# Optimization experiments

Hardware: AMD Instinct MI355X
Metric: run time of the kernel (lower is better)

Reference implementation:

```python
import jax, jax.numpy as jnp
import numpy as np

B, H, C, PX, PY = 2, 16, 4, 16, 16
EXTRA = 64
HD = 64
N = C * PX * PY + EXTRA


def setup_inputs() -> dict:
    key = jax.random.key(0)
    ks = jax.random.split(key, 8)
    q = jax.random.normal(ks[0], (B, H, N, HD), jnp.float32)
    k = jax.random.normal(ks[1], (B, H, N, HD), jnp.float32)
    v = jax.random.normal(ks[2], (B, H, N, HD), jnp.float32)
    # valid SE(3) world-to-camera matrices: rotation via QR (det fixed to +1)
    A = jax.random.normal(ks[3], (B, C, 3, 3), jnp.float32)
    Q, _ = jnp.linalg.qr(A)
    det = jnp.linalg.det(Q)
    Q = Q * det[..., None, None]
    t = 0.5 * jax.random.normal(ks[4], (B, C, 3), jnp.float32)
    top = jnp.concatenate([Q, t[..., None]], -1)
    bot = jnp.broadcast_to(jnp.array([0.0, 0.0, 0.0, 1.0], jnp.float32), (B, C, 1, 4))
    viewmats = jnp.concatenate([top, bot], -2)
    # pinhole intrinsics (no skew)
    fx = 300.0 + 10.0 * jax.random.uniform(ks[5], (B, C))
    fy = 300.0 + 10.0 * jax.random.uniform(ks[6], (B, C))
    z = jnp.zeros((B, C)); o = jnp.ones((B, C))
    cx = 128.0 * o; cy = 128.0 * o
    Ks = jnp.stack([jnp.stack([fx, z, cx], -1), jnp.stack([z, fy, cy], -1), jnp.stack([z, z, o], -1)], -2)
    spatial_mask = jnp.arange(N) >= EXTRA  # first EXTRA tokens are non-spatial
    return {"q": q, "k": k, "v": v, "viewmats": viewmats, "Ks": Ks,
            "spatial_mask": spatial_mask, "patches_x": PX, "patches_y": PY,
            "image_width": 256, "image_height": 256}


def _invert_SE3(T):
    R = T[..., :3, :3]; t = T[..., :3, 3]
    Rinv = jnp.swapaxes(R, -1, -2)
    tinv = -jnp.einsum('...ij,...j->...i', Rinv, t)
    top = jnp.concatenate([Rinv, tinv[..., None]], -1)
    bot = jnp.broadcast_to(jnp.array([0.0, 0.0, 0.0, 1.0], T.dtype), T.shape[:-2] + (1, 4))
    return jnp.concatenate([top, bot], -2)


def _lift(K3):
    out = jnp.zeros(K3.shape[:-2] + (4, 4), K3.dtype)
    return out.at[..., :3, :3].set(K3).at[..., 3, 3].set(1.0)


def _invert_K(K):
    fx = K[..., 0, 0]; fy = K[..., 1, 1]; cx = K[..., 0, 2]; cy = K[..., 1, 2]
    z = jnp.zeros_like(fx); o = jnp.ones_like(fx)
    return jnp.stack([jnp.stack([1.0 / fx, z, -cx / fx], -1),
                      jnp.stack([z, 1.0 / fy, -cy / fy], -1),
                      jnp.stack([z, z, o], -1)], -2)


def _transform(feats, M, cosx, sinx, cosy, siny, inverse):
    # Block-diagonal: [tiled 4x4 projmat on D/2 | RoPE-x on D/4 | RoPE-y on D/4]
    Bq, Hq, Nq, D = feats.shape
    h2 = D // 2; h4 = D // 4
    p = feats[..., :h2].reshape(Bq, Hq, Nq, h2 // 4, 4)
    p = jnp.einsum('bnij,bhnkj->bhnki', M, p).reshape(Bq, Hq, Nq, h2)

    def rope(x, c, s):
        c = c[None, None]; s = s[None, None]  # [1,1,N,nf]
        xa, xb = x[..., : x.shape[-1] // 2], x[..., x.shape[-1] // 2:]
        if inverse:
            return jnp.concatenate([c * xa - s * xb, s * xa + c * xb], -1)
        return jnp.concatenate([c * xa + s * xb, -s * xa + c * xb], -1)

    rx = rope(feats[..., h2:h2 + h4], cosx, sinx)
    ry = rope(feats[..., h2 + h4:], cosy, siny)
    return jnp.concatenate([p, rx, ry], -1)


def reference(q, k, v, viewmats, Ks, spatial_mask, patches_x, patches_y, image_width, image_height):
    D = q.shape[-1]
    Bq, Cq = viewmats.shape[:2]
    # normalized intrinsics
    fx = Ks[..., 0, 0] / image_width; fy = Ks[..., 1, 1] / image_height
    cx = Ks[..., 0, 2] / image_width - 0.5; cy = Ks[..., 1, 2] / image_height - 0.5
    z = jnp.zeros_like(fx); o = jnp.ones_like(fx)
    Kn = jnp.stack([jnp.stack([fx, z, cx], -1), jnp.stack([z, fy, cy], -1), jnp.stack([z, z, o], -1)], -2)
    P = jnp.einsum('...ij,...jk->...ik', _lift(Kn), viewmats)          # [B,C,4,4]
    P_T = jnp.swapaxes(P, -1, -2)
    P_inv = jnp.einsum('...ij,...jk->...ik', _invert_SE3(viewmats), _lift(_invert_K(Kn)))
    # RoPE tables over spatial tokens (split convention, base=100, scale=1)
    nf = D // 8
    freqs = 100.0 ** (-jnp.arange(nf, dtype=jnp.float32) / nf)
    pos_x = jnp.tile(jnp.arange(patches_x, dtype=jnp.float32), patches_y * Cq)
    pos_y = jnp.tile(jnp.repeat(jnp.arange(patches_y, dtype=jnp.float32), patches_x), Cq)
    ang_x = pos_x[:, None] * freqs; ang_y = pos_y[:, None] * freqs  # [S,nf]
    mask = spatial_mask
    S = pos_x.shape[0]
    # index of each token within the spatial-token ordering (masked scatter, vectorized)
    sidx = jnp.clip(jnp.cumsum(mask.astype(jnp.int32)) - 1, 0, S - 1)
    m = mask[:, None]
    cosx = jnp.where(m, jnp.cos(ang_x)[sidx], 1.0); sinx = jnp.where(m, jnp.sin(ang_x)[sidx], 0.0)
    cosy = jnp.where(m, jnp.cos(ang_y)[sidx], 1.0); siny = jnp.where(m, jnp.sin(ang_y)[sidx], 0.0)
    cam = sidx // (patches_x * patches_y)  # camera id per token
    I4 = jnp.eye(4, dtype=q.dtype)
    mm = mask[None, :, None, None]
    Mq = jnp.where(mm, P_T[:, cam], I4)    # [B,N,4,4]
    Mkv = jnp.where(mm, P_inv[:, cam], I4)
    Mo = jnp.where(mm, P[:, cam], I4)
    qt = _transform(q, Mq, cosx, sinx, cosy, siny, False)
    kt = _transform(k, Mkv, cosx, sinx, cosy, siny, False)
    vt = _transform(v, Mkv, cosx, sinx, cosy, siny, False)
    logits = jnp.einsum('bhqd,bhkd->bhqk', qt, kt) / jnp.sqrt(jnp.float32(D))
    attn = jax.nn.softmax(logits, axis=-1)
    out = jnp.einsum('bhqk,bhkd->bhqd', attn, vt)
    return _transform(out, Mo, cosx, sinx, cosy, siny, True)
```

## Files before the change

### kernel.cpp

```cpp
#include <hip/hip_runtime.h>
#include <math.h>

typedef _Float16 f16;
typedef _Float16 f16x8 __attribute__((ext_vector_type(8)));
typedef __fp16 h16x2 __attribute__((ext_vector_type(2)));
typedef float f32x16 __attribute__((ext_vector_type(16)));
typedef unsigned int u32;
typedef u32 u32x4 __attribute__((ext_vector_type(4)));

constexpr int Bc = 2, Hc = 16, Cc = 4, PXc = 16, PYc = 16, EXTRAc = 64, HDc = 64;
constexpr int Nc = Cc * PXc * PYc + EXTRAc;
constexpr int BH = Bc * Hc;
constexpr int KT = 64;
constexpr int NKT = Nc / KT;
constexpr int KS = 4;

constexpr size_t TENS_SZ  = (size_t)BH * Nc * HDc * 2;
constexpr size_t QF_OFF   = 0;
constexpr size_t KF_OFF   = QF_OFF + TENS_SZ;
constexpr size_t VT_OFF   = KF_OFF + TENS_SZ;
constexpr size_t PART_OFF = VT_OFF + TENS_SZ;
constexpr size_t ML_OFF   = PART_OFF + (size_t)KS * TENS_SZ;

__device__ const float FREQS[8] = {1.0f, 0.5623413252f, 0.31622776601f, 0.17782794100f,
                                   0.1f, 0.05623413252f, 0.031622776602f, 0.017782794100f};
constexpr float QSCALE = 0.125f * 1.4426950408889634f;

__device__ __forceinline__ void compute_M(float* M, const float* __restrict__ vm,
                                          const float* __restrict__ Ks3, int b, int cam, int which) {
    const float* V  = vm + (b * Cc + cam) * 16;
    const float* K3 = Ks3 + (b * Cc + cam) * 9;
    float fx = K3[0] * (1.0f / 256.0f);
    float fy = K3[4] * (1.0f / 256.0f);
    float cx = K3[2] * (1.0f / 256.0f) - 0.5f;
    float cy = K3[5] * (1.0f / 256.0f) - 0.5f;
    if (which == 2) {
        float IV[16];
        IV[0] = V[0]; IV[1] = V[4]; IV[2] = V[8];
        IV[4] = V[1]; IV[5] = V[5]; IV[6] = V[9];
        IV[8] = V[2]; IV[9] = V[6]; IV[10] = V[10];
        float tx = V[3], ty = V[7], tz = V[11];
        IV[3]  = -(IV[0] * tx + IV[1] * ty + IV[2] * tz);
        IV[7]  = -(IV[4] * tx + IV[5] * ty + IV[6] * tz);
        IV[11] = -(IV[8] * tx + IV[9] * ty + IV[10] * tz);
        IV[12] = 0.f; IV[13] = 0.f; IV[14] = 0.f; IV[15] = 1.f;
        float ifx = 1.f / fx, ify = 1.f / fy;
        float ncx = -cx * ifx, ncy = -cy * ify;
        #pragma unroll
        for (int i = 0; i < 4; ++i) {
            M[i * 4 + 0] = IV[i * 4 + 0] * ifx;
            M[i * 4 + 1] = IV[i * 4 + 1] * ify;
            M[i * 4 + 2] = IV[i * 4 + 0] * ncx + IV[i * 4 + 1] * ncy + IV[i * 4 + 2];
            M[i * 4 + 3] = IV[i * 4 + 3];
        }
    } else {
        float P[16];
        #pragma unroll
        for (int j = 0; j < 4; ++j) {
            P[0 * 4 + j] = fx * V[0 * 4 + j] + cx * V[2 * 4 + j];
            P[1 * 4 + j] = fy * V[1 * 4 + j] + cy * V[2 * 4 + j];
            P[2 * 4 + j] = V[2 * 4 + j];
            P[3 * 4 + j] = V[3 * 4 + j];
        }
        if (which == 0) {
            #pragma unroll
            for (int i = 0; i < 16; ++i) M[i] = P[i];
        } else {
            #pragma unroll
            for (int i = 0; i < 4; ++i)
                #pragma unroll
                for (int j = 0; j < 4; ++j) M[i * 4 + j] = P[j * 4 + i];
        }
    }
}

template <bool INV>
__device__ __forceinline__ void xf_seg(float* v16, int seg, int n, int b, int which,
                                       const float* __restrict__ vm, const float* __restrict__ Ks3) {
    if (n < EXTRAc) return;
    int sidx = n - EXTRAc;
    int cam = sidx >> 8;
    if (seg < 2) {
        float M[16];
        compute_M(M, vm, Ks3, b, cam, which);
        #pragma unroll
        for (int g = 0; g < 4; ++g) {
            float a0 = v16[4 * g], a1 = v16[4 * g + 1], a2 = v16[4 * g + 2], a3 = v16[4 * g + 3];
            v16[4 * g + 0] = M[0]  * a0 + M[1]  * a1 + M[2]  * a2 + M[3]  * a3;
            v16[4 * g + 1] = M[4]  * a0 + M[5]  * a1 + M[6]  * a2 + M[7]  * a3;
            v16[4 * g + 2] = M[8]  * a0 + M[9]  * a1 + M[10] * a2 + M[11] * a3;
            v16[4 * g + 3] = M[12] * a0 + M[13] * a1 + M[14] * a2 + M[15] * a3;
        }
    } else {
        float pos = (seg == 2) ? (float)(sidx & (PXc - 1)) : (float)((sidx >> 4) & (PYc - 1));
        #pragma unroll
        for (int f = 0; f < 8; ++f) {
            float s, c;
            __sincosf(pos * FREQS[f], &s, &c);
            float xa = v16[f], xb = v16[8 + f];
            if (INV) {
                v16[f]     = c * xa - s * xb;
                v16[8 + f] = s * xa + c * xb;
            } else {
                v16[f]     = c * xa + s * xb;
                v16[8 + f] = -s * xa + c * xb;
            }
        }
    }
}

__device__ __forceinline__ u32 pkh(float a, float b) {
    h16x2 r = __builtin_amdgcn_cvt_pkrtz(a, b);
    return __builtin_bit_cast(u32, r);
}

__device__ __forceinline__ void gld16(const void* g, void* l) {
    __builtin_amdgcn_global_load_lds((const __attribute__((address_space(1))) unsigned int*)g,
                                     (__attribute__((address_space(3))) unsigned int*)l, 16, 0, 0);
}

__device__ __forceinline__ f32x16 zero16() {
    f32x16 z = {0.f,0.f,0.f,0.f,0.f,0.f,0.f,0.f,0.f,0.f,0.f,0.f,0.f,0.f,0.f,0.f};
    return z;
}

__global__ void prope_xform_kernel(const float* __restrict__ q, const float* __restrict__ k,
                                   const float* __restrict__ v,
                                   const float* __restrict__ viewmats, const float* __restrict__ Ks,
                                   char* __restrict__ wsb) {
    __shared__ f16 tile[64][72];
    if (blockIdx.x < 1088) {
        int id = blockIdx.x * 256 + threadIdx.x;
        int seg = id & 3;
        int rid = id >> 2;
        int tensor = rid / (BH * Nc);
        int row = rid - tensor * (BH * Nc);
        int n = row % Nc;
        int b = (row / Nc) >> 4;
        const float* src = (tensor ? k : q) + (size_t)row * 64 + seg * 16;
        float vals[16];
        #pragma unroll
        for (int i = 0; i < 4; ++i) ((float4*)vals)[i] = ((const float4*)src)[i];
        xf_seg<false>(vals, seg, n, b, tensor ? 2 : 1, viewmats, Ks);
        float scale = tensor ? 1.0f : QSCALE;
        f16 o[16];
        #pragma unroll
        for (int i = 0; i < 16; ++i) o[i] = (f16)(vals[i] * scale);
        if (tensor == 0) {
            char* dst = wsb + QF_OFF + (size_t)row * 128 + seg * 32;
            ((float4*)dst)[0] = ((float4*)o)[0];
            ((float4*)dst)[1] = ((float4*)o)[1];
        } else {
            int r = n & 63;
            char* base = wsb + KF_OFF + (size_t)row * 128;
            *(float4*)(base + 16 * ((2 * seg)     ^ (r & 7))) = ((float4*)o)[0];
            *(float4*)(base + 16 * ((2 * seg + 1) ^ (r & 7))) = ((float4*)o)[1];
        }
    } else {
        int vb = blockIdx.x - 1088;
        int kt = vb >> 5, bh = vb & 31;
        int b = bh >> 4;
        int t = threadIdx.x;
        {
            int r = t >> 2, seg = t & 3;
            int n = kt * 64 + r;
            const float* src = v + ((size_t)bh * Nc + n) * 64 + seg * 16;
            float vals[16];
            #pragma unroll
            for (int i = 0; i < 4; ++i) ((float4*)vals)[i] = ((const float4*)src)[i];
            xf_seg<false>(vals, seg, n, b, 2, viewmats, Ks);
            #pragma unroll
            for (int i = 0; i < 16; ++i) tile[r][seg * 16 + i] = (f16)vals[i];
        }
        __syncthreads();
        {
            int d = t >> 2, ks = t & 3;
            f16 o[16];
            #pragma unroll
            for (int j = 0; j < 16; ++j) o[j] = tile[ks * 16 + j][d];
            char* base = wsb + VT_OFF + (((size_t)bh * 64 + d) * Nc + kt * 64) * 2;
            *(float4*)(base + 16 * ((2 * ks)     ^ (d & 7))) = ((float4*)o)[0];
            *(float4*)(base + 16 * ((2 * ks + 1) ^ (d & 7))) = ((float4*)o)[1];
        }
    }
}

__global__ __launch_bounds__(128, 3) void prope_attn_mfma_kernel(
    const char* __restrict__ wsb, char* __restrict__ partO, float* __restrict__ partML) {
    __shared__ char smem[32768];

    const int tid = threadIdx.x;
    const int wv = tid >> 6, lane = tid & 63;
    const int q = lane & 31, h = lane >> 5;
    const int qt = blockIdx.x, bh = blockIdx.y, z = blockIdx.z;
    const int ts = (NKT * z) / KS, te = (NKT * (z + 1)) / KS;
    const int qrow = qt * 64 + wv * 32 + q;

    const char* kfb = wsb + KF_OFF + (size_t)bh * Nc * 128;
    const char* vtb = wsb + VT_OFF + (size_t)bh * 64 * (Nc * 2);
    const char* qfb = wsb + QF_OFF + ((size_t)bh * Nc + qrow) * 128;

    f16x8 qb[4];
    #pragma unroll
    for (int c = 0; c < 4; ++c) qb[c] = *(const f16x8*)(qfb + c * 32 + h * 16);

    auto stage = [&](int bsel, int t) {
        char* dst = smem + bsel * 16384 + (wv ? 8192 : 0);
        if (wv == 0) {
            const char* src = kfb + (size_t)t * 8192;
            #pragma unroll
            for (int j = 0; j < 8; ++j)
                gld16(src + j * 1024 + lane * 16, dst + j * 1024);
        } else {
            const char* src = vtb + t * 128 + (lane & 7) * 16;
            #pragma unroll
            for (int j = 0; j < 8; ++j)
                gld16(src + (size_t)(j * 8 + (lane >> 3)) * (Nc * 2), dst + j * 1024);
        }
    };

    f32x16 o0 = zero16(), o1 = zero16();
    float mrun = -1e30f, lrun = 0.f;

    stage(0, ts);
    __syncthreads();

    for (int it = ts; it < te; ++it) {
        const int cur = (it - ts) & 1;
        if (it + 1 < te) stage(cur ^ 1, it + 1);
        const char* kb = smem + cur * 16384;
        const char* vb = kb + 8192;

        f32x16 s0 = zero16(), s1 = zero16();
        #pragma unroll
        for (int c = 0; c < 4; ++c) {
            int col = c * 32 + h * 16;
            int r0 = q, r1 = 32 + q;
            f16x8 a0 = *(const f16x8*)(kb + ((r0 * 128 + col) ^ ((r0 & 7) << 4)));
            f16x8 a1 = *(const f16x8*)(kb + ((r1 * 128 + col) ^ ((r1 & 7) << 4)));
            s0 = __builtin_amdgcn_mfma_f32_32x32x16_f16(a0, qb[c], s0, 0, 0, 0);
            s1 = __builtin_amdgcn_mfma_f32_32x32x16_f16(a1, qb[c], s1, 0, 0, 0);
        }

        float tm = -1e30f;
        #pragma unroll
        for (int i = 0; i < 16; ++i) { tm = fmaxf(tm, s0[i]); tm = fmaxf(tm, s1[i]); }
        tm = fmaxf(tm, __shfl_xor(tm, 32, 64));
        float nm = fmaxf(mrun, tm);
        float corr = exp2f(mrun - nm);
        mrun = nm;
        float p0[16], p1[16];
        float ps = 0.f;
        #pragma unroll
        for (int i = 0; i < 16; ++i) { p0[i] = exp2f(s0[i] - nm); ps += p0[i]; }
        #pragma unroll
        for (int i = 0; i < 16; ++i) { p1[i] = exp2f(s1[i] - nm); ps += p1[i]; }
        ps += __shfl_xor(ps, 32, 64);
        lrun = lrun * corr + ps;
        #pragma unroll
        for (int i = 0; i < 16; ++i) { o0[i] *= corr; o1[i] *= corr; }

        u32 U0[8], U1[8];
        #pragma unroll
        for (int g = 0; g < 4; ++g) {
            U0[g * 2 + 0] = pkh(p0[4 * g + 0], p0[4 * g + 1]);
            U0[g * 2 + 1] = pkh(p0[4 * g + 2], p0[4 * g + 3]);
            U1[g * 2 + 0] = pkh(p1[4 * g + 0], p1[4 * g + 1]);
            U1[g * 2 + 1] = pkh(p1[4 * g + 2], p1[4 * g + 3]);
        }

        #pragma unroll
        for (int c = 0; c < 4; ++c) {
            const u32* Us = (c < 2) ? U0 : U1;
            int gl = 2 * (c & 1);
            u32 x0 = Us[(gl + 1) * 2 + 0], x1 = Us[(gl + 1) * 2 + 1];
            u32 y0 = Us[gl * 2 + 0],       y1 = Us[gl * 2 + 1];
            u32 s0w = h ? y0 : x0;
            u32 s1w = h ? y1 : x1;
            u32 r0 = (u32)__shfl_xor((int)s0w, 32, 64);
            u32 r1 = (u32)__shfl_xor((int)s1w, 32, 64);
            u32 own0 = h ? x0 : y0, own1 = h ? x1 : y1;
            u32 w0 = h ? r0 : own0;
            u32 w1 = h ? r1 : own1;
            u32 w2 = h ? own0 : r0;
            u32 w3 = h ? own1 : r1;
            u32x4 fw = {w0, w1, w2, w3};
            f16x8 pb = __builtin_bit_cast(f16x8, fw);
            int col = c * 32 + h * 16;
            int r0r = q, r1r = 32 + q;
            f16x8 va0 = *(const f16x8*)(vb + ((r0r * 128 + col) ^ ((r0r & 7) << 4)));
            f16x8 va1 = *(const f16x8*)(vb + ((r1r * 128 + col) ^ ((r1r & 7) << 4)));
            o0 = __builtin_amdgcn_mfma_f32_32x32x16_f16(va0, pb, o0, 0, 0, 0);
            o1 = __builtin_amdgcn_mfma_f32_32x32x16_f16(va1, pb, o1, 0, 0, 0);
        }
        __syncthreads();
    }

    float invl = 1.f / lrun;
    char* ob = smem;
    int row = wv * 32 + q;
    #pragma unroll
    for (int g = 0; g < 4; ++g) {
        #pragma unroll
        for (int w = 0; w < 2; ++w) {
            u32 u0 = pkh(o0[4 * g + 2 * w] * invl, o0[4 * g + 2 * w + 1] * invl);
            u32 u1 = pkh(o1[4 * g + 2 * w] * invl, o1[4 * g + 2 * w + 1] * invl);
            int col0 = 16 * g + 8 * h + 4 * w;
            *(u32*)(ob + ((row * 128 + col0) ^ ((row & 7) << 4))) = u0;
            *(u32*)(ob + ((row * 128 + col0 + 64) ^ ((row & 7) << 4))) = u1;
        }
    }
    if (h == 0) {
        float2 mlv = {mrun, lrun};
        ((float2*)partML)[((size_t)z * BH + bh) * Nc + qt * 64 + row] = mlv;
    }
    __syncthreads();
    {
        int r = tid >> 1, half = tid & 1;
        char* dst = partO + (((size_t)z * BH + bh) * Nc + qt * 64 + r) * 128 + half * 64;
        #pragma unroll
        for (int j = 0; j < 4; ++j) {
            float4 val = *(float4*)(ob + ((r * 128 + half * 64 + j * 16) ^ ((r & 7) << 4)));
            ((float4*)dst)[j] = val;
        }
    }
}

__global__ void prope_combine_kernel(const char* __restrict__ wsb,
                                     const float* __restrict__ viewmats, const float* __restrict__ Ks,
                                     float* __restrict__ out) {
    int id = blockIdx.x * 256 + threadIdx.x;
    int seg = id & 3, rid = id >> 2;
    int n = rid % Nc, bh = rid / Nc, b = bh >> 4;
    const float2* ml = (const float2*)(wsb + ML_OFF);
    float m[KS], l[KS];
    float mstar = -1e30f;
    #pragma unroll
    for (int s = 0; s < KS; ++s) {
        float2 v = ml[((size_t)s * BH + bh) * Nc + n];
        m[s] = v.x; l[s] = v.y;
        mstar = fmaxf(mstar, m[s]);
    }
    float wsum = 0.f, wgt[KS];
    #pragma unroll
    for (int s = 0; s < KS; ++s) { wgt[s] = exp2f(m[s] - mstar) * l[s]; wsum += wgt[s]; }
    float inv = 1.f / wsum;
    float acc[16];
    #pragma unroll
    for (int i = 0; i < 16; ++i) acc[i] = 0.f;
    #pragma unroll
    for (int s = 0; s < KS; ++s) {
        const char* op = wsb + PART_OFF + (((size_t)s * BH + bh) * Nc + n) * 128 + seg * 32;
        f16x8 a0 = *(const f16x8*)op;
        f16x8 a1 = *(const f16x8*)(op + 16);
        #pragma unroll
        for (int i = 0; i < 8; ++i) acc[i] += wgt[s] * (float)a0[i];
        #pragma unroll
        for (int i = 0; i < 8; ++i) acc[8 + i] += wgt[s] * (float)a1[i];
    }
    #pragma unroll
    for (int i = 0; i < 16; ++i) acc[i] *= inv;
    xf_seg<true>(acc, seg, n, b, 0, viewmats, Ks);
    float* go = out + ((size_t)bh * Nc + n) * 64 + seg * 16;
    #pragma unroll
    for (int i = 0; i < 4; ++i) ((float4*)go)[i] = ((const float4*)acc)[i];
}

extern "C" void kernel_launch(void* const* d_in, const int* in_sizes, int n_in,
                              void* d_out, int out_size, void* d_ws, size_t ws_size,
                              hipStream_t stream) {
    const float* q        = (const float*)d_in[0];
    const float* k        = (const float*)d_in[1];
    const float* v        = (const float*)d_in[2];
    const float* viewmats = (const float*)d_in[3];
    const float* Ks       = (const float*)d_in[4];
    char* wsb  = (char*)d_ws;
    float* out = (float*)d_out;

    prope_xform_kernel<<<1088 + 544, 256, 0, stream>>>(q, k, v, viewmats, Ks, wsb);
    prope_attn_mfma_kernel<<<dim3(NKT, BH, KS), 128, 0, stream>>>(wsb, wsb + PART_OFF,
                                                                  (float*)(wsb + ML_OFF));
    prope_combine_kernel<<<(BH * Nc * 4) / 256, 256, 0, stream>>>(wsb, viewmats, Ks, out);
}
```

Baseline: 54.88 us.

## Pre-swizzle Q/K/V into MFMA fragment layout and load directly to registers

The transform kernel now writes Q, K and V^T in a layout matching MFMA operand fragments, so each lane loads its operands with coalesced 16-byte global loads. The attention kernel drops the LDS double-buffered staging and its barriers, using one wave per 32-query tile, which doubles the grid. This removes LDS traffic and synchronisation but relies on L2/cache hits for K/V reuse across query tiles and loses explicit prefetch overlap.

```diff
diff --git a/kernel.cpp b/kernel.cpp
--- a/kernel.cpp
+++ b/kernel.cpp
@@ -14,8 +14,10 @@
 constexpr int KT = 64;
 constexpr int NKT = Nc / KT;
 constexpr int KS = 4;
+constexpr int NQT = Nc / 32;
 
 constexpr size_t TENS_SZ  = (size_t)BH * Nc * HDc * 2;
+constexpr size_t PBH      = (size_t)Nc * 128;
 constexpr size_t QF_OFF   = 0;
 constexpr size_t KF_OFF   = QF_OFF + TENS_SZ;
 constexpr size_t VT_OFF   = KF_OFF + TENS_SZ;
@@ -114,11 +116,6 @@
     return __builtin_bit_cast(u32, r);
 }
 
-__device__ __forceinline__ void gld16(const void* g, void* l) {
-    __builtin_amdgcn_global_load_lds((const __attribute__((address_space(1))) unsigned int*)g,
-                                     (__attribute__((address_space(3))) unsigned int*)l, 16, 0, 0);
-}
-
 __device__ __forceinline__ f32x16 zero16() {
     f32x16 z = {0.f,0.f,0.f,0.f,0.f,0.f,0.f,0.f,0.f,0.f,0.f,0.f,0.f,0.f,0.f,0.f};
     return z;
@@ -136,7 +133,8 @@
         int tensor = rid / (BH * Nc);
         int row = rid - tensor * (BH * Nc);
         int n = row % Nc;
-        int b = (row / Nc) >> 4;
+        int bhq = row / Nc;
+        int b = bhq >> 4;
         const float* src = (tensor ? k : q) + (size_t)row * 64 + seg * 16;
         float vals[16];
         #pragma unroll
@@ -147,14 +145,15 @@
         #pragma unroll
         for (int i = 0; i < 16; ++i) o[i] = (f16)(vals[i] * scale);
         if (tensor == 0) {
-            char* dst = wsb + QF_OFF + (size_t)row * 128 + seg * 32;
-            ((float4*)dst)[0] = ((float4*)o)[0];
-            ((float4*)dst)[1] = ((float4*)o)[1];
+            char* base = wsb + QF_OFF + (size_t)bhq * PBH + (size_t)(n >> 5) * 4096;
+            int qq = n & 31;
+            *(float4*)(base + (seg * 2 + 0) * 512 + qq * 16) = ((float4*)o)[0];
+            *(float4*)(base + (seg * 2 + 1) * 512 + qq * 16) = ((float4*)o)[1];
         } else {
-            int r = n & 63;
-            char* base = wsb + KF_OFF + (size_t)row * 128;
-            *(float4*)(base + 16 * ((2 * seg)     ^ (r & 7))) = ((float4*)o)[0];
-            *(float4*)(base + 16 * ((2 * seg + 1) ^ (r & 7))) = ((float4*)o)[1];
+            char* base = wsb + KF_OFF + (size_t)bhq * PBH + (size_t)(n >> 6) * 8192;
+            int kk = n & 63, rh = kk >> 5, qq = kk & 31;
+            *(float4*)(base + (((seg * 2 + rh) * 2 + 0) * 32 + qq) * 16) = ((float4*)o)[0];
+            *(float4*)(base + (((seg * 2 + rh) * 2 + 1) * 32 + qq) * 16) = ((float4*)o)[1];
         }
     } else {
         int vb = blockIdx.x - 1088;
@@ -178,68 +177,57 @@
             f16 o[16];
             #pragma unroll
             for (int j = 0; j < 16; ++j) o[j] = tile[ks * 16 + j][d];
-            char* base = wsb + VT_OFF + (((size_t)bh * 64 + d) * Nc + kt * 64) * 2;
-            *(float4*)(base + 16 * ((2 * ks)     ^ (d & 7))) = ((float4*)o)[0];
-            *(float4*)(base + 16 * ((2 * ks + 1) ^ (d & 7))) = ((float4*)o)[1];
-        }
-    }
-}
-
-__global__ __launch_bounds__(128, 3) void prope_attn_mfma_kernel(
+            int dh = d >> 5, dq = d & 31;
+            char* base = wsb + VT_OFF + (size_t)bh * PBH + (size_t)kt * 8192;
+            *(float4*)(base + (((ks * 2 + dh) * 2 + 0) * 32 + dq) * 16) = ((float4*)o)[0];
+            *(float4*)(base + (((ks * 2 + dh) * 2 + 1) * 32 + dq) * 16) = ((float4*)o)[1];
+        }
+    }
+}
+
+__global__ __launch_bounds__(64, 3) void prope_attn_mfma_kernel(
     const char* __restrict__ wsb, char* __restrict__ partO, float* __restrict__ partML) {
-    __shared__ char smem[32768];
-
-    const int tid = threadIdx.x;
-    const int wv = tid >> 6, lane = tid & 63;
+    __shared__ char ob[4096];
+
+    const int lane = threadIdx.x;
     const int q = lane & 31, h = lane >> 5;
     const int qt = blockIdx.x, bh = blockIdx.y, z = blockIdx.z;
     const int ts = (NKT * z) / KS, te = (NKT * (z + 1)) / KS;
-    const int qrow = qt * 64 + wv * 32 + q;
-
-    const char* kfb = wsb + KF_OFF + (size_t)bh * Nc * 128;
-    const char* vtb = wsb + VT_OFF + (size_t)bh * 64 * (Nc * 2);
-    const char* qfb = wsb + QF_OFF + ((size_t)bh * Nc + qrow) * 128;
+
+    const char* kfb = wsb + KF_OFF + (size_t)bh * PBH;
+    const char* vfb = wsb + VT_OFF + (size_t)bh * PBH;
+    const char* qfb = wsb + QF_OFF + (size_t)bh * PBH + (size_t)qt * 4096;
 
     f16x8 qb[4];
     #pragma unroll
-    for (int c = 0; c < 4; ++c) qb[c] = *(const f16x8*)(qfb + c * 32 + h * 16);
-
-    auto stage = [&](int bsel, int t) {
-        char* dst = smem + bsel * 16384 + (wv ? 8192 : 0);
-        if (wv == 0) {
-            const char* src = kfb + (size_t)t * 8192;
-            #pragma unroll
-            for (int j = 0; j < 8; ++j)
-                gld16(src + j * 1024 + lane * 16, dst + j * 1024);
-        } else {
-            const char* src = vtb + t * 128 + (lane & 7) * 16;
-            #pragma unroll
-            for (int j = 0; j < 8; ++j)
-                gld16(src + (size_t)(j * 8 + (lane >> 3)) * (Nc * 2), dst + j * 1024);
-        }
-    };
+    for (int c = 0; c < 4; ++c) qb[c] = *(const f16x8*)(qfb + c * 1024 + lane * 16);
 
     f32x16 o0 = zero16(), o1 = zero16();
     float mrun = -1e30f, lrun = 0.f;
 
-    stage(0, ts);
-    __syncthreads();
-
     for (int it = ts; it < te; ++it) {
-        const int cur = (it - ts) & 1;
-        if (it + 1 < te) stage(cur ^ 1, it + 1);
-        const char* kb = smem + cur * 16384;
-        const char* vb = kb + 8192;
+        const char* kb = kfb + (size_t)it * 8192;
+        const char* vb = vfb + (size_t)it * 8192;
+
+        f16x8 ka0[4], ka1[4];
+        #pragma unroll
+        for (int c = 0; c < 4; ++c) {
+            ka0[c] = *(const f16x8*)(kb + (c * 2 + 0) * 1024 + lane * 16);
+            ka1[c] = *(const f16x8*)(kb + (c * 2 + 1) * 1024 + lane * 16);
+        }
 
         f32x16 s0 = zero16(), s1 = zero16();
         #pragma unroll
         for (int c = 0; c < 4; ++c) {
-            int col = c * 32 + h * 16;
-            int r0 = q, r1 = 32 + q;
-            f16x8 a0 = *(const f16x8*)(kb + ((r0 * 128 + col) ^ ((r0 & 7) << 4)));
-            f16x8 a1 = *(const f16x8*)(kb + ((r1 * 128 + col) ^ ((r1 & 7) << 4)));
-            s0 = __builtin_amdgcn_mfma_f32_32x32x16_f16(a0, qb[c], s0, 0, 0, 0);
-            s1 = __builtin_amdgcn_mfma_f32_32x32x16_f16(a1, qb[c], s1, 0, 0, 0);
+            s0 = __builtin_amdgcn_mfma_f32_32x32x16_f16(ka0[c], qb[c], s0, 0, 0, 0);
+            s1 = __builtin_amdgcn_mfma_f32_32x32x16_f16(ka1[c], qb[c], s1, 0, 0, 0);
+        }
+
+        f16x8 va0[4], va1[4];
+        #pragma unroll
+        for (int c = 0; c < 4; ++c) {
+            va0[c] = *(const f16x8*)(vb + (c * 2 + 0) * 1024 + lane * 16);
+            va1[c] = *(const f16x8*)(vb + (c * 2 + 1) * 1024 + lane * 16);
         }
 
         float tm = -1e30f;
@@ -286,19 +274,12 @@
             u32 w3 = h ? own1 : r1;
             u32x4 fw = {w0, w1, w2, w3};
             f16x8 pb = __builtin_bit_cast(f16x8, fw);
-            int col = c * 32 + h * 16;
-            int r0r = q, r1r = 32 + q;
-            f16x8 va0 = *(const f16x8*)(vb + ((r0r * 128 + col) ^ ((r0r & 7) << 4)));
-            f16x8 va1 = *(const f16x8*)(vb + ((r1r * 128 + col) ^ ((r1r & 7) << 4)));
-            o0 = __builtin_amdgcn_mfma_f32_32x32x16_f16(va0, pb, o0, 0, 0, 0);
-            o1 = __builtin_amdgcn_mfma_f32_32x32x16_f16(va1, pb, o1, 0, 0, 0);
-        }
-        __syncthreads();
+            o0 = __builtin_amdgcn_mfma_f32_32x32x16_f16(va0[c], pb, o0, 0, 0, 0);
+            o1 = __builtin_amdgcn_mfma_f32_32x32x16_f16(va1[c], pb, o1, 0, 0, 0);
+        }
     }
 
     float invl = 1.f / lrun;
-    char* ob = smem;
-    int row = wv * 32 + q;
     #pragma unroll
     for (int g = 0; g < 4; ++g) {
         #pragma unroll
@@ -306,18 +287,18 @@
             u32 u0 = pkh(o0[4 * g + 2 * w] * invl, o0[4 * g + 2 * w + 1] * invl);
             u32 u1 = pkh(o1[4 * g + 2 * w] * invl, o1[4 * g + 2 * w + 1] * invl);
             int col0 = 16 * g + 8 * h + 4 * w;
-            *(u32*)(ob + ((row * 128 + col0) ^ ((row & 7) << 4))) = u0;
-            *(u32*)(ob + ((row * 128 + col0 + 64) ^ ((row & 7) << 4))) = u1;
+            *(u32*)(ob + ((q * 128 + col0) ^ ((q & 7) << 4))) = u0;
+            *(u32*)(ob + ((q * 128 + col0 + 64) ^ ((q & 7) << 4))) = u1;
         }
     }
     if (h == 0) {
         float2 mlv = {mrun, lrun};
-        ((float2*)partML)[((size_t)z * BH + bh) * Nc + qt * 64 + row] = mlv;
+        ((float2*)partML)[((size_t)z * BH + bh) * Nc + qt * 32 + q] = mlv;
     }
     __syncthreads();
     {
-        int r = tid >> 1, half = tid & 1;
-        char* dst = partO + (((size_t)z * BH + bh) * Nc + qt * 64 + r) * 128 + half * 64;
+        int r = lane >> 1, half = lane & 1;
+        char* dst = partO + (((size_t)z * BH + bh) * Nc + qt * 32 + r) * 128 + half * 64;
         #pragma unroll
         for (int j = 0; j < 4; ++j) {
             float4 val = *(float4*)(ob + ((r * 128 + half * 64 + j * 16) ^ ((r & 7) << 4)));
@@ -378,7 +359,7 @@
     float* out = (float*)d_out;
 
     prope_xform_kernel<<<1088 + 544, 256, 0, stream>>>(q, k, v, viewmats, Ks, wsb);
-    prope_attn_mfma_kernel<<<dim3(NKT, BH, KS), 128, 0, stream>>>(wsb, wsb + PART_OFF,
-                                                                  (float*)(wsb + ML_OFF));
+    prope_attn_mfma_kernel<<<dim3(NQT, BH, KS), 64, 0, stream>>>(wsb, wsb + PART_OFF,
+                                                                 (float*)(wsb + ML_OFF));
     prope_combine_kernel<<<(BH * Nc * 4) / 256, 256, 0, stream>>>(wsb, viewmats, Ks, out);
 }
```

Result: faster. 48.03 us (-12.5%).
